# Performance work log

Hardware: AMD Instinct MI355X
Metric: run time of the kernel (lower is better)

## Reference

```python
import jax, jax.numpy as jnp
import numpy as np

SR = 48000
SECONDS = 2.0
T = int(SECONDS * SR)  # 96000 samples


def _shift(x, n):
    """Delay 1-D signal x by n samples, zero-filling (n may be a traced int >= 0)."""
    t = jnp.arange(x.shape[0])
    return jnp.where(t >= n, jnp.roll(x, n), jnp.zeros((), x.dtype))


def setup_inputs() -> dict:
    key = jax.random.key(0)
    k1, k2 = jax.random.split(key)
    excitation = jax.random.normal(k1, (T,), dtype=jnp.float32)
    pluckPosition = jax.random.uniform(k2, (1,), dtype=jnp.float32, minval=0.1, maxval=0.9)
    return {
        "length": 240,  # delay-line length in samples -> f0 = SR/length = 200 Hz
        "pluckPosition": pluckPosition,
        "excitation": excitation,
        "nut_gain": jnp.asarray(-0.99, jnp.float32),    # GuitarNuts reflection
        "bridge_gain": jnp.asarray(-0.995, jnp.float32),  # GuitarBridge reflection
        "bridge_b": jnp.asarray(0.5, jnp.float32),      # bridge one-zero lowpass coeff
        "disp_a": jnp.asarray(0.3, jnp.float32),        # dispersion FIR coeff
    }


def reference(length, pluckPosition, excitation, nut_gain, bridge_gain, bridge_b, disp_a):
    L = int(length)
    pluck = pluckPosition[0]
    nUp = jnp.round(L * pluck).astype(jnp.int32)   # StringSegment(nUp)
    nDown = jnp.int32(L) - nUp                      # StringSegment(nDown)

    def bridge_lp(x):
        # one-zero lowpass at the bridge: y[t] = (1-b)*x[t] + b*x[t-1]
        return (1.0 - bridge_b) * x + bridge_b * _shift(x, 1)

    def dispersion(x):
        # two-tap FIR dispersion filter: y[t] = a*x[t] + (1-a)*x[t-1]
        return disp_a * x + (1.0 - disp_a) * _shift(x, 1)

    def vibrate(l, r):
        # right-going wave: up segment -> dispersion -> down segment
        r2 = _shift(dispersion(_shift(r, nUp)), nDown)
        # left-going wave: down segment -> dispersion -> up segment
        l2 = _shift(dispersion(_shift(l, nDown)), nUp)
        return l2, r2

    # _start: inject excitation (split between the two traveling waves at pluck point)
    left0 = _shift(0.5 * excitation, nDown)
    right0 = _shift(0.5 * excitation, nUp)

    n_iter = T // L  # len(excitation) // int(length)

    def step(carry, _):
        l, r, acc = carry
        r_new = nut_gain * l                      # _lterminate: nut reflection of left wave
        l_new = bridge_gain * bridge_lp(r)        # _rterminate: bridge reflection of right wave
        l_new, r_new = vibrate(l_new, r_new)      # _vibrate: propagate through segments
        return (l_new, r_new, acc + l_new + r_new), None

    acc0 = left0 + right0
    (_, _, acc), _ = jax.lax.scan(step, (left0, right0, acc0), None, length=n_iter)
    return acc  # sum(left_signal) + sum(right_signal), shape [T]
```

## Files before the change

kernel.cpp:

```cpp
#include <hip/hip_runtime.h>


#define PREP_BLK 1024
#define SPAN_MAX 4640
#define SEQ_BLK  512
#define TAP_LO   5

template<int NA, int NB>
static __device__ __forceinline__ void convT(const float* a, const float* b, float* c) {
#pragma unroll
    for (int i = 0; i < NA + NB - 1; ++i) c[i] = 0.f;
#pragma unroll
    for (int i = 0; i < NA; ++i)
#pragma unroll
        for (int j = 0; j < NB; ++j) c[i + j] += a[i] * b[j];
}

struct Base {
    int L, nUp, nDown;
    float gb, gn, g;
    float c0, c1, c2, d0, d1;
    float e[4];
};

static __device__ __forceinline__ Base mkbase(const int* Lp, const float* pk,
        const float* gnp, const float* gbp, const float* bbp, const float* dap) {
    Base b;
    b.L = Lp[0];
    b.gn = gnp[0]; b.gb = gbp[0];
    const float bb = bbp[0], da = dap[0];
    b.nUp   = (int)rintf((float)b.L * pk[0]);
    b.nDown = b.L - b.nUp;
    b.c0 = da * (1.f - bb);
    b.c1 = da * bb + (1.f - da) * (1.f - bb);
    b.c2 = (1.f - da) * bb;
    b.d0 = da; b.d1 = 1.f - da;
    b.e[0] = b.c0*b.d0;
    b.e[1] = b.c0*b.d1 + b.c1*b.d0;
    b.e[2] = b.c1*b.d1 + b.c2*b.d0;
    b.e[3] = b.c2*b.d1;
    b.g = b.gb * b.gn;
    return b;
}

__global__ __launch_bounds__(PREP_BLK, 1)
void prep_kernel(const int* Lp, const float* pk, const float* __restrict__ exc,
                 const float* gnp, const float* gbp, const float* bbp, const float* dap,
                 float* __restrict__ D4l, float* __restrict__ D4r, int T) {
    __shared__ float Dls[SPAN_MAX];
    __shared__ float Drs[SPAN_MAX];

    const Base B = mkbase(Lp, pk, gnp, gbp, bbp, dap);
    float p2[7], p3[10], p4[13], p5[16], p6[19], p7[22];
    convT<4,4>(B.e, B.e, p2);
    convT<7,4>(p2, B.e, p3);
    convT<7,7>(p2, p2, p4);
    convT<13,4>(p4, B.e, p5);
    convT<13,7>(p4, p2, p6);
    convT<13,10>(p4, p3, p7);
    const float g = B.g, g2 = g*g, g3 = g2*g, g4 = g2*g2, g5 = g4*g, g6 = g4*g2, g7 = g4*g3;

    const int P0   = 2 * B.L;
    const int H    = 7 * P0 + 21;
    const int span = PREP_BLK + H;
    const int t0   = blockIdx.x * PREP_BLK;
    const int base = t0 - H;

    const int mx = (B.nUp > B.nDown) ? B.nUp : B.nDown;
    const bool safe = (base - B.L - mx - 2) >= 0;

    for (int j = threadIdx.x; j < span; j += PREP_BLK) {
        const int s = base + j;
        float dl, dr;
        if (safe) {
            dl = 0.5f * exc[s - B.nDown]
               + (0.5f * B.gb) * (B.c0 * exc[s - B.L     - B.nUp]
                                + B.c1 * exc[s - B.L - 1 - B.nUp]
                                + B.c2 * exc[s - B.L - 2 - B.nUp]);
            dr = 0.5f * exc[s - B.nUp]
               + (0.5f * B.gn) * (B.d0 * exc[s - B.L     - B.nDown]
                                + B.d1 * exc[s - B.L - 1 - B.nDown]);
        } else {
            auto ex = [&](int i) -> float { return (i >= 0) ? exc[i] : 0.f; };
            if (s < 0) { dl = 0.f; dr = 0.f; }
            else {
                dl = 0.5f * ex(s - B.nDown)
                   + (0.5f * B.gb) * (B.c0 * ex(s - B.L     - B.nUp)
                                    + B.c1 * ex(s - B.L - 1 - B.nUp)
                                    + B.c2 * ex(s - B.L - 2 - B.nUp));
                dr = 0.5f * ex(s - B.nUp)
                   + (0.5f * B.gn) * (B.d0 * ex(s - B.L     - B.nDown)
                                    + B.d1 * ex(s - B.L - 1 - B.nDown));
            }
        }
        Dls[j] = dl; Drs[j] = dr;
    }
    __syncthreads();

    const int t = t0 + threadIdx.x;
    if (t < T) {
        const int p = H + threadIdx.x;
        float al = Dls[p], ar = Drs[p];
#pragma unroll
        for (int k = 0; k < 4;  ++k) { const int j = p -     P0 - k; const float w = g  * B.e[k]; al += w*Dls[j]; ar += w*Drs[j]; }
#pragma unroll
        for (int k = 0; k < 7;  ++k) { const int j = p - 2 * P0 - k; const float w = g2 * p2[k];  al += w*Dls[j]; ar += w*Drs[j]; }
#pragma unroll
        for (int k = 0; k < 10; ++k) { const int j = p - 3 * P0 - k; const float w = g3 * p3[k];  al += w*Dls[j]; ar += w*Drs[j]; }
#pragma unroll
        for (int k = 0; k < 13; ++k) { const int j = p - 4 * P0 - k; const float w = g4 * p4[k];  al += w*Dls[j]; ar += w*Drs[j]; }
#pragma unroll
        for (int k = 0; k < 16; ++k) { const int j = p - 5 * P0 - k; const float w = g5 * p5[k];  al += w*Dls[j]; ar += w*Drs[j]; }
#pragma unroll
        for (int k = 0; k < 19; ++k) { const int j = p - 6 * P0 - k; const float w = g6 * p6[k];  al += w*Dls[j]; ar += w*Drs[j]; }
#pragma unroll
        for (int k = 0; k < 22; ++k) { const int j = p - 7 * P0 - k; const float w = g7 * p7[k];  al += w*Dls[j]; ar += w*Drs[j]; }
        D4l[t] = al; D4r[t] = ar;
    }
}

__global__ __launch_bounds__(SEQ_BLK, 1)
void seq_kernel(const int* Lp, const float* pk, const float* gnp, const float* gbp,
                const float* bbp, const float* dap,
                float* __restrict__ Slw, float* __restrict__ Srw, int T) {
    __shared__ float4 pl[2][2][512];
    __shared__ float4 pre[4][6];

    const Base B = mkbase(Lp, pk, gnp, gbp, bbp, dap);
    float p2[7], p4[13], f[25];
    convT<4,4>(B.e, B.e, p2);
    convT<7,7>(p2, p2, p4);
    convT<13,13>(p4, p4, f);
    const float g2 = B.g * B.g, g4 = g2 * g2, G = g4 * g4;

    const int L = B.L, P = 16 * L, NA = 2 * L;
    const int lam = threadIdx.x;
    const bool act = lam < NA;
    float* __restrict__ DD = blockIdx.x ? Srw : Slw;

    {   float4* z = &pl[0][0][0];
        for (int i = lam; i < 2*2*512; i += SEQ_BLK) z[i] = float4{0,0,0,0};
        if (lam < 24) (&pre[0][0])[lam] = float4{0,0,0,0};
    }
    __syncthreads();

    const int nphase = (T + P - 1) / P;

    auto load8 = [&](int t, float4& a, float4& b) {
        if (t + 8 <= T) {
            a = *(const float4*)(DD + t); b = *(const float4*)(DD + t + 4);
        } else {
            float tmp[8];
#pragma unroll
            for (int s = 0; s < 8; ++s) tmp[s] = (t + s < T) ? DD[t + s] : 0.f;
            a = float4{tmp[0],tmp[1],tmp[2],tmp[3]};
            b = float4{tmp[4],tmp[5],tmp[6],tmp[7]};
        }
    };

    float4 dE[2] = {{0,0,0,0},{0,0,0,0}};
    float4 dO[2] = {{0,0,0,0},{0,0,0,0}};
    if (act)               load8(lam << 3,       dE[0], dE[1]);
    if (act && nphase > 1) load8(P + (lam << 3), dO[0], dO[1]);

    float4 pS0{0,0,0,0}, pS1{0,0,0,0};

    auto do_phase = [&](int q, float4 (&dv)[2]) {
        const int par = q & 1, pp = par ^ 1, rs = (q + 2) & 3, wsl = q & 3;

        float4 W0{0,0,0,0}, W1{0,0,0,0}, W2{0,0,0,0},
               W3{0,0,0,0}, W4{0,0,0,0}, W5{0,0,0,0};
        if (act) {
            if (lam >= 3) {
                W0 = pl[pp][0][lam-3]; W1 = pl[pp][1][lam-3];
                W2 = pl[pp][0][lam-2]; W3 = pl[pp][1][lam-2];
                W4 = pl[pp][0][lam-1]; W5 = pl[pp][1][lam-1];
            } else if (lam == 2) {
                W0 = pre[rs][4]; W1 = pre[rs][5];
                W2 = pl[pp][0][0]; W3 = pl[pp][1][0];
                W4 = pl[pp][0][1]; W5 = pl[pp][1][1];
            } else if (lam == 1) {
                W0 = pre[rs][2]; W1 = pre[rs][3];
                W2 = pre[rs][4]; W3 = pre[rs][5];
                W4 = pl[pp][0][0]; W5 = pl[pp][1][0];
            } else {
                W0 = pre[rs][0]; W1 = pre[rs][1];
                W2 = pre[rs][2]; W3 = pre[rs][3];
                W4 = pre[rs][4]; W5 = pre[rs][5];
            }
        }

        float S[8];
        if (act) {
            const float cw[32] = {W0.x,W0.y,W0.z,W0.w, W1.x,W1.y,W1.z,W1.w,
                                  W2.x,W2.y,W2.z,W2.w, W3.x,W3.y,W3.z,W3.w,
                                  W4.x,W4.y,W4.z,W4.w, W5.x,W5.y,W5.z,W5.w,
                                  pS0.x,pS0.y,pS0.z,pS0.w, pS1.x,pS1.y,pS1.z,pS1.w};
            const float dvf[8] = {dv[0].x,dv[0].y,dv[0].z,dv[0].w,
                                  dv[1].x,dv[1].y,dv[1].z,dv[1].w};
#pragma unroll
            for (int s = 0; s < 8; ++s) {
                float a0 = 0.f, a1 = 0.f, a2 = 0.f, a3 = 0.f;
#pragma unroll
                for (int j = 0; j < 5; ++j) {
                    const int k = TAP_LO + 4 * j;
                    a0 += f[k    ] * cw[24 + s - k    ];
                    a1 += f[k + 1] * cw[24 + s - k - 1];
                    a2 += f[k + 2] * cw[24 + s - k - 2];
                    a3 += f[k + 3] * cw[24 + s - k - 3];
                }
                S[s] = dvf[s] + G * ((a0 + a1) + (a2 + a3));
            }
            pS0 = float4{S[0],S[1],S[2],S[3]};
            pS1 = float4{S[4],S[5],S[6],S[7]};

            pl[par][0][lam] = pS0; pl[par][1][lam] = pS1;
            if (lam == NA - 3) { pre[wsl][0] = pS0; pre[wsl][1] = pS1; }
            if (lam == NA - 2) { pre[wsl][2] = pS0; pre[wsl][3] = pS1; }
            if (lam == NA - 1) { pre[wsl][4] = pS0; pre[wsl][5] = pS1; }
        }

        if (act && (q + 2) < nphase) load8((q + 2) * P + (lam << 3), dv[0], dv[1]);

        if (act) {
            const int tg = q * P + (lam << 3);
            if (tg + 8 <= T) {
                *(float4*)(DD + tg)     = pS0;
                *(float4*)(DD + tg + 4) = pS1;
            } else {
#pragma unroll
                for (int s = 0; s < 8; ++s) if (tg + s < T) DD[tg + s] = S[s];
            }
        }

        __builtin_amdgcn_sched_barrier(0);
        asm volatile("s_waitcnt lgkmcnt(0)");
        __builtin_amdgcn_s_barrier();
        __builtin_amdgcn_sched_barrier(0);
    };

    int q = 0;
    for (; q + 1 < nphase; q += 2) { do_phase(q, dE); do_phase(q + 1, dO); }
    if (q < nphase) do_phase(q, dE);
}

__global__ void add_kernel(const float* __restrict__ a, const float* __restrict__ b,
                           float* __restrict__ o, int T) {
    const int i = (blockIdx.x * blockDim.x + threadIdx.x) * 4;
    if (i + 4 <= T) {
        const float4 x = *(const float4*)(a + i);
        const float4 y = *(const float4*)(b + i);
        *(float4*)(o + i) = float4{x.x + y.x, x.y + y.y, x.z + y.z, x.w + y.w};
    } else if (i < T) {
        for (int s = i; s < T; ++s) o[s] = a[s] + b[s];
    }
}

extern "C" void kernel_launch(void* const* d_in, const int* in_sizes, int n_in,
                              void* d_out, int out_size, void* d_ws, size_t ws_size,
                              hipStream_t stream) {
    const int*   Lp  = (const int*)  d_in[0];
    const float* pk  = (const float*)d_in[1];
    const float* exc = (const float*)d_in[2];
    const float* gn  = (const float*)d_in[3];
    const float* gb  = (const float*)d_in[4];
    const float* bb  = (const float*)d_in[5];
    const float* da  = (const float*)d_in[6];
    float* out = (float*)d_out;
    float* D4l = (float*)d_ws;
    float* D4r = D4l + out_size;
    const int T = out_size;

    prep_kernel<<<(T + PREP_BLK - 1) / PREP_BLK, PREP_BLK, 0, stream>>>(
        Lp, pk, exc, gn, gb, bb, da, D4l, D4r, T);
    seq_kernel<<<2, SEQ_BLK, 0, stream>>>(Lp, pk, gn, gb, bb, da, D4l, D4r, T);
    add_kernel<<<(T / 4 + 255) / 256, 256, 0, stream>>>(D4l, D4r, out, T);
}
```

Before: 52.59 us.

## Replace sequential recurrence scan with parallel multi-pass FIR expansion

Replaces the two-block sequential phase recurrence with a parallel scheme. Powers of the per-period filter are precomputed (composite filters for lags 1..16 periods), and the recurrence is unrolled into three fully parallel convolution passes over the whole signal, with the final pass fusing the left/right add. This removes the long serial dependency chain that ran on only two workgroups, at the cost of more total FLOPs and several extra kernel launches and global round trips.

```diff
diff --git a/kernel.cpp b/kernel.cpp
--- a/kernel.cpp
+++ b/kernel.cpp
@@ -3,8 +3,6 @@
 
 #define PREP_BLK 1024
 #define SPAN_MAX 4640
-#define SEQ_BLK  512
-#define TAP_LO   5
 
 template<int NA, int NB>
 static __device__ __forceinline__ void convT(const float* a, const float* b, float* c) {
@@ -119,141 +117,146 @@
     }
 }
 
-__global__ __launch_bounds__(SEQ_BLK, 1)
-void seq_kernel(const int* Lp, const float* pk, const float* gnp, const float* gbp,
-                const float* bbp, const float* dap,
-                float* __restrict__ Slw, float* __restrict__ Srw, int T) {
-    __shared__ float4 pl[2][2][512];
-    __shared__ float4 pre[4][6];
-
+__global__ __launch_bounds__(512, 1)
+void filtergen_kernel(const int* Lp, const float* pk, const float* gnp, const float* gbp,
+                      const float* bbp, const float* dap, float* __restrict__ FIL) {
+    __shared__ float E[1200];
     const Base B = mkbase(Lp, pk, gnp, gbp, bbp, dap);
-    float p2[7], p4[13], f[25];
-    convT<4,4>(B.e, B.e, p2);
-    convT<7,7>(p2, p2, p4);
-    convT<13,13>(p4, p4, f);
-    const float g2 = B.g * B.g, g4 = g2 * g2, G = g4 * g4;
-
-    const int L = B.L, P = 16 * L, NA = 2 * L;
-    const int lam = threadIdx.x;
-    const bool act = lam < NA;
-    float* __restrict__ DD = blockIdx.x ? Srw : Slw;
-
-    {   float4* z = &pl[0][0][0];
-        for (int i = lam; i < 2*2*512; i += SEQ_BLK) z[i] = float4{0,0,0,0};
-        if (lam < 24) (&pre[0][0])[lam] = float4{0,0,0,0};
-    }
-    __syncthreads();
-
-    const int nphase = (T + P - 1) / P;
-
-    auto load8 = [&](int t, float4& a, float4& b) {
-        if (t + 8 <= T) {
-            a = *(const float4*)(DD + t); b = *(const float4*)(DD + t + 4);
-        } else {
-            float tmp[8];
-#pragma unroll
-            for (int s = 0; s < 8; ++s) tmp[s] = (t + s < T) ? DD[t + s] : 0.f;
-            a = float4{tmp[0],tmp[1],tmp[2],tmp[3]};
-            b = float4{tmp[4],tmp[5],tmp[6],tmp[7]};
+    const int tid = threadIdx.x;
+
+    if (tid < 4) E[tid] = B.e[tid];
+
+    auto cstep = [&](int ao, int na, int bo, int nb, int co) {
+        __syncthreads();
+        const int nc = na + nb - 1;
+        for (int j = tid; j < nc; j += 512) {
+            float s = 0.f;
+            const int ilo = (j - nb + 1 > 0) ? j - nb + 1 : 0;
+            const int ihi = (j < na - 1) ? j : na - 1;
+            for (int i = ilo; i <= ihi; ++i) s += E[ao + i] * E[bo + j - i];
+            E[co + j] = s;
         }
     };
-
-    float4 dE[2] = {{0,0,0,0},{0,0,0,0}};
-    float4 dO[2] = {{0,0,0,0},{0,0,0,0}};
-    if (act)               load8(lam << 3,       dE[0], dE[1]);
-    if (act && nphase > 1) load8(P + (lam << 3), dO[0], dO[1]);
-
-    float4 pS0{0,0,0,0}, pS1{0,0,0,0};
-
-    auto do_phase = [&](int q, float4 (&dv)[2]) {
-        const int par = q & 1, pp = par ^ 1, rs = (q + 2) & 3, wsl = q & 3;
-
-        float4 W0{0,0,0,0}, W1{0,0,0,0}, W2{0,0,0,0},
-               W3{0,0,0,0}, W4{0,0,0,0}, W5{0,0,0,0};
-        if (act) {
-            if (lam >= 3) {
-                W0 = pl[pp][0][lam-3]; W1 = pl[pp][1][lam-3];
-                W2 = pl[pp][0][lam-2]; W3 = pl[pp][1][lam-2];
-                W4 = pl[pp][0][lam-1]; W5 = pl[pp][1][lam-1];
-            } else if (lam == 2) {
-                W0 = pre[rs][4]; W1 = pre[rs][5];
-                W2 = pl[pp][0][0]; W3 = pl[pp][1][0];
-                W4 = pl[pp][0][1]; W5 = pl[pp][1][1];
-            } else if (lam == 1) {
-                W0 = pre[rs][2]; W1 = pre[rs][3];
-                W2 = pre[rs][4]; W3 = pre[rs][5];
-                W4 = pl[pp][0][0]; W5 = pl[pp][1][0];
-            } else {
-                W0 = pre[rs][0]; W1 = pre[rs][1];
-                W2 = pre[rs][2]; W3 = pre[rs][3];
-                W4 = pre[rs][4]; W5 = pre[rs][5];
-            }
-        }
-
-        float S[8];
-        if (act) {
-            const float cw[32] = {W0.x,W0.y,W0.z,W0.w, W1.x,W1.y,W1.z,W1.w,
-                                  W2.x,W2.y,W2.z,W2.w, W3.x,W3.y,W3.z,W3.w,
-                                  W4.x,W4.y,W4.z,W4.w, W5.x,W5.y,W5.z,W5.w,
-                                  pS0.x,pS0.y,pS0.z,pS0.w, pS1.x,pS1.y,pS1.z,pS1.w};
-            const float dvf[8] = {dv[0].x,dv[0].y,dv[0].z,dv[0].w,
-                                  dv[1].x,dv[1].y,dv[1].z,dv[1].w};
-#pragma unroll
-            for (int s = 0; s < 8; ++s) {
-                float a0 = 0.f, a1 = 0.f, a2 = 0.f, a3 = 0.f;
-#pragma unroll
-                for (int j = 0; j < 5; ++j) {
-                    const int k = TAP_LO + 4 * j;
-                    a0 += f[k    ] * cw[24 + s - k    ];
-                    a1 += f[k + 1] * cw[24 + s - k - 1];
-                    a2 += f[k + 2] * cw[24 + s - k - 2];
-                    a3 += f[k + 3] * cw[24 + s - k - 3];
-                }
-                S[s] = dvf[s] + G * ((a0 + a1) + (a2 + a3));
-            }
-            pS0 = float4{S[0],S[1],S[2],S[3]};
-            pS1 = float4{S[4],S[5],S[6],S[7]};
-
-            pl[par][0][lam] = pS0; pl[par][1][lam] = pS1;
-            if (lam == NA - 3) { pre[wsl][0] = pS0; pre[wsl][1] = pS1; }
-            if (lam == NA - 2) { pre[wsl][2] = pS0; pre[wsl][3] = pS1; }
-            if (lam == NA - 1) { pre[wsl][4] = pS0; pre[wsl][5] = pS1; }
-        }
-
-        if (act && (q + 2) < nphase) load8((q + 2) * P + (lam << 3), dv[0], dv[1]);
-
-        if (act) {
-            const int tg = q * P + (lam << 3);
-            if (tg + 8 <= T) {
-                *(float4*)(DD + tg)     = pS0;
-                *(float4*)(DD + tg + 4) = pS1;
-            } else {
-#pragma unroll
-                for (int s = 0; s < 8; ++s) if (tg + s < T) DD[tg + s] = S[s];
-            }
-        }
-
-        __builtin_amdgcn_sched_barrier(0);
-        asm volatile("s_waitcnt lgkmcnt(0)");
-        __builtin_amdgcn_s_barrier();
-        __builtin_amdgcn_sched_barrier(0);
-    };
-
-    int q = 0;
-    for (; q + 1 < nphase; q += 2) { do_phase(q, dE); do_phase(q + 1, dO); }
-    if (q < nphase) do_phase(q, dE);
-}
-
-__global__ void add_kernel(const float* __restrict__ a, const float* __restrict__ b,
-                           float* __restrict__ o, int T) {
-    const int i = (blockIdx.x * blockDim.x + threadIdx.x) * 4;
-    if (i + 4 <= T) {
-        const float4 x = *(const float4*)(a + i);
-        const float4 y = *(const float4*)(b + i);
-        *(float4*)(o + i) = float4{x.x + y.x, x.y + y.y, x.z + y.z, x.w + y.w};
-    } else if (i < T) {
-        for (int s = i; s < T; ++s) o[s] = a[s] + b[s];
-    }
+    cstep(0,4,    0,4,    8);
+    cstep(8,7,    8,7,    16);
+    cstep(16,13,  16,13,  32);
+    cstep(32,25,  32,25,  64);
+    cstep(64,49,  32,25,  120);
+    cstep(64,49,  64,49,  200);
+    cstep(200,97, 200,97, 304);
+    cstep(304,193,200,97, 504);
+    cstep(304,193,304,193,800);
+    __syncthreads();
+
+    const float g = B.g, g2 = g*g, g4 = g2*g2, G = g4*g4;
+    const float G2 = G*G, G3 = G2*G, G4 = G2*G2, G8 = G4*G4, G12 = G8*G4, G16 = G8*G8;
+
+    for (int j = tid; j < 25;  j += 512) FIL[   0 + j] = G   * E[32  + j];
+    for (int j = tid; j < 49;  j += 512) FIL[  64 + j] = G2  * E[64  + j];
+    for (int j = tid; j < 73;  j += 512) FIL[ 128 + j] = G3  * E[120 + j];
+    for (int j = tid; j < 97;  j += 512) FIL[ 256 + j] = G4  * E[200 + j];
+    for (int j = tid; j < 193; j += 512) FIL[ 384 + j] = G8  * E[304 + j];
+    for (int j = tid; j < 289; j += 512) FIL[ 640 + j] = G12 * E[504 + j];
+    for (int j = tid; j < 385; j += 512) FIL[1024 + j] = G16 * E[800 + j];
+}
+
+template<int SAMP, int MAXT>
+__global__ __launch_bounds__(256, 2)
+void pass_kernel(const float* __restrict__ fil,
+                 const float* __restrict__ inL, float* __restrict__ outL,
+                 const float* __restrict__ inR, float* __restrict__ outR,
+                 const int* __restrict__ Lp, int T,
+                 int k0, int o0, int n0, int k1, int o1, int n1, int k2, int o2, int n2) {
+    constexpr int CH = 256 * SAMP;
+    __shared__ float W[3][CH + MAXT + 4];
+    __shared__ float F[3][MAXT + 4];
+
+    const int P8 = 16 * Lp[0];
+    const float* __restrict__ X = blockIdx.y ? inR : inL;
+    float* __restrict__ O       = blockIdx.y ? outR : outL;
+    const int b0 = blockIdx.x * CH;
+    const int ks[3] = {k0, k1, k2}, os[3] = {o0, o1, o2}, ns[3] = {n0, n1, n2};
+
+    bool on[3];
+#pragma unroll
+    for (int i = 0; i < 3; ++i) {
+        const int taps = ns[i];
+        on[i] = (b0 + CH - 1 - ks[i] * P8) >= 0;
+        if (!on[i]) continue;
+        const int w0  = b0 - ks[i] * P8 - (taps - 1);
+        const int len = CH + taps - 1;
+        for (int idx = threadIdx.x; idx < len; idx += 256) {
+            const int s = w0 + idx;
+            W[i][idx] = (s >= 0 && s < T) ? X[s] : 0.f;
+        }
+        for (int j = threadIdx.x; j < taps; j += 256) F[i][j] = fil[os[i] + j];
+    }
+    __syncthreads();
+
+    const int t0 = b0 + threadIdx.x * SAMP;
+    float acc[SAMP];
+#pragma unroll
+    for (int s = 0; s < SAMP; ++s) { const int t = t0 + s; acc[s] = (t < T) ? X[t] : 0.f; }
+
+#pragma unroll
+    for (int i = 0; i < 3; ++i) {
+        if (!on[i]) continue;
+        const int taps = ns[i];
+        const int base = threadIdx.x * SAMP + taps - 1;
+#pragma unroll 4
+        for (int j = 0; j < taps; ++j) {
+            const float fv = F[i][j];
+#pragma unroll
+            for (int s = 0; s < SAMP; ++s) acc[s] += fv * W[i][base + s - j];
+        }
+    }
+#pragma unroll
+    for (int s = 0; s < SAMP; ++s) { const int t = t0 + s; if (t < T) O[t] = acc[s]; }
+}
+
+template<int SAMP>
+__global__ __launch_bounds__(256, 2)
+void pass3_kernel(const float* __restrict__ fil,
+                  const float* __restrict__ inL, const float* __restrict__ inR,
+                  float* __restrict__ out, const int* __restrict__ Lp, int T,
+                  int kk, int oo, int nn) {
+    constexpr int CH = 256 * SAMP;
+    __shared__ float WL[CH + 388], WR[CH + 388], F[388];
+
+    const int P8 = 16 * Lp[0];
+    const int b0 = blockIdx.x * CH;
+    const int taps = nn;
+    const bool on = (b0 + CH - 1 - kk * P8) >= 0;
+    if (on) {
+        const int w0 = b0 - kk * P8 - (taps - 1), len = CH + taps - 1;
+        for (int idx = threadIdx.x; idx < len; idx += 256) {
+            const int s = w0 + idx;
+            const bool ok = (s >= 0 && s < T);
+            WL[idx] = ok ? inL[s] : 0.f;
+            WR[idx] = ok ? inR[s] : 0.f;
+        }
+        for (int j = threadIdx.x; j < taps; j += 256) F[j] = fil[oo + j];
+    }
+    __syncthreads();
+
+    const int t0 = b0 + threadIdx.x * SAMP;
+    float acc[SAMP];
+#pragma unroll
+    for (int s = 0; s < SAMP; ++s) {
+        const int t = t0 + s;
+        acc[s] = (t < T) ? (inL[t] + inR[t]) : 0.f;
+    }
+    if (on) {
+        const int base = threadIdx.x * SAMP + taps - 1;
+#pragma unroll 4
+        for (int j = 0; j < taps; ++j) {
+            const float fv = F[j];
+#pragma unroll
+            for (int s = 0; s < SAMP; ++s) acc[s] += fv * (WL[base + s - j] + WR[base + s - j]);
+        }
+    }
+#pragma unroll
+    for (int s = 0; s < SAMP; ++s) { const int t = t0 + s; if (t < T) out[t] = acc[s]; }
 }
 
 extern "C" void kernel_launch(void* const* d_in, const int* in_sizes, int n_in,
@@ -267,12 +270,22 @@
     const float* bb  = (const float*)d_in[5];
     const float* da  = (const float*)d_in[6];
     float* out = (float*)d_out;
-    float* D4l = (float*)d_ws;
-    float* D4r = D4l + out_size;
     const int T = out_size;
 
+    float* R0  = (float*)d_ws;
+    float* R1  = R0 + T;
+    float* R2  = R0 + 2 * T;
+    float* FIL = R0 + 3 * T;
+    float* D   = out;
+
+    filtergen_kernel<<<1, 512, 0, stream>>>(Lp, pk, gn, gb, bb, da, FIL);
     prep_kernel<<<(T + PREP_BLK - 1) / PREP_BLK, PREP_BLK, 0, stream>>>(
-        Lp, pk, exc, gn, gb, bb, da, D4l, D4r, T);
-    seq_kernel<<<2, SEQ_BLK, 0, stream>>>(Lp, pk, gn, gb, bb, da, D4l, D4r, T);
-    add_kernel<<<(T / 4 + 255) / 256, 256, 0, stream>>>(D4l, D4r, out, T);
-}
+        Lp, pk, exc, gn, gb, bb, da, R0, R1, T);
+
+    pass_kernel<8, 80><<<dim3((T + 2047) / 2048, 2), 256, 0, stream>>>(
+        FIL, R0, R2, R1, D, Lp, T, 1, 0, 25, 2, 64, 49, 3, 128, 73);
+    pass_kernel<4, 292><<<dim3((T + 1023) / 1024, 2), 256, 0, stream>>>(
+        FIL, R2, R0, D, R1, Lp, T, 4, 256, 97, 8, 384, 193, 12, 640, 289);
+    pass3_kernel<2><<<(T + 511) / 512, 256, 0, stream>>>(
+        FIL, R0, R1, out, Lp, T, 16, 1024, 385);
+}
```

Measured after the change: 117.2 us. +122.9%, slower.
